# Kernel tuning notes

Measured on AMD Instinct MI355X. Metric: run time of the kernel, lower is better.

## Reference

```python
import jax, jax.numpy as jnp
import numpy as np

IN_DIM = 1024
OUT_DIM = 1024
NHEAD = 16
K = 9  # template(1032) - dim(1024) + 1


def _slinear(vec, template, conv_w, conv_b, lin_b):
    # Conv2d over template produces the [out_dim, in_dim] weight matrix.
    w = jax.lax.conv_general_dilated(
        template, conv_w, window_strides=(1, 1), padding='VALID',
        dimension_numbers=('NCHW', 'OIHW', 'NCHW'))  # [1,1,out_dim,in_dim]
    w = w[0, 0] + conv_b  # broadcast conv bias (scalar per out-channel)
    return vec @ w.T + lin_b  # F.linear(vec, w) + bias


def setup_inputs() -> dict:
    key = jax.random.key(0)
    ks = jax.random.split(key, 13)
    S, B = 2048, 2
    d = {
        'query': jax.random.normal(ks[0], (S, B, IN_DIM), jnp.float32),
        'key': jax.random.normal(ks[1], (S, B, IN_DIM), jnp.float32),
        'value': jax.random.normal(ks[2], (S, B, IN_DIM), jnp.float32),
        'template': jax.random.normal(ks[3], (1, 1, 1032, 1032), jnp.float32),
    }
    for i, name in enumerate(['wq', 'wk', 'wv']):
        d[name + '_cw'] = jax.random.normal(ks[4 + 3 * i], (1, 1, K, K), jnp.float32) * 0.05
        d[name + '_cb'] = jax.random.normal(ks[5 + 3 * i], (1,), jnp.float32) * 0.05
        d[name + '_b'] = jax.random.normal(ks[6 + 3 * i], (OUT_DIM,), jnp.float32) * 0.05
    return d


def reference(query, key, value, template,
              wq_cw, wq_cb, wq_b, wk_cw, wk_cb, wk_b, wv_cw, wv_cb, wv_b):
    q = _slinear(query, template, wq_cw, wq_cb, wq_b)
    k = _slinear(key, template, wk_cw, wk_cb, wk_b)
    v = _slinear(value, template, wv_cw, wv_cb, wv_b)
    S, B = q.shape[0], q.shape[1]
    h_dim = OUT_DIM // NHEAD
    scale = h_dim ** 0.5
    qh = q.reshape(S, B, NHEAD, h_dim)
    kh = k.reshape(S, B, NHEAD, h_dim)
    vh = v.reshape(S, B, NHEAD, h_dim)
    # batch_first=False path: scores then softmax over last dim
    scores = jnp.einsum('ibhd,jbhd->bhij', qh, kh) / scale  # [B,H,S,S]
    attn = jax.nn.softmax(scores, axis=-1)
    out = jnp.einsum('bhij,jbhd->ibhd', attn, vh).reshape(S, B, OUT_DIM)
    return out
```

## Files before the change

### kernel.cpp

```cpp
#include <hip/hip_runtime.h>
#include <math.h>

#define TDIM   1032
#define DIM    1024
#define SLEN   2048
#define BATCH  2
#define NROWS  (SLEN*BATCH)
#define NHEAD  16
#define HD     64

typedef unsigned short u16;
typedef short short8 __attribute__((ext_vector_type(8)));
typedef short bf16x4 __attribute__((ext_vector_type(4)));
typedef float f32x4  __attribute__((ext_vector_type(4)));

#define CSCALE 0.18033688011112042f

__device__ inline unsigned fbits(float x) {
    union { float f; unsigned u; } v; v.f = x; return v.u;
}
__device__ inline float asfloat(unsigned u) {
    union { unsigned u; float f; } v; v.u = u; return v.f;
}
__device__ inline u16 f2bf_rne(float x) {
    unsigned u = fbits(x);
    unsigned r = u + 0x7fffu + ((u >> 16) & 1u);
    return (u16)(r >> 16);
}
__device__ inline float bf2f(u16 b) { return asfloat(((unsigned)b) << 16); }
__device__ inline void dma16(const u16* g, u16* l) {
    __builtin_amdgcn_global_load_lds(
        (const __attribute__((address_space(1))) void*)g,
        (__attribute__((address_space(3))) void*)l, 16, 0, 0);
}

__global__ __launch_bounds__(256) void conv_weight_kernel(
    const float* __restrict__ tmpl,
    const float* __restrict__ cw0, const float* __restrict__ cb0,
    const float* __restrict__ cw1, const float* __restrict__ cb1,
    const float* __restrict__ cw2, const float* __restrict__ cb2,
    u16* __restrict__ Wh, u16* __restrict__ Wl)
{
    int t = blockIdx.z;
    const float* cw = (t == 0) ? cw0 : ((t == 1) ? cw1 : cw2);
    const float* cb = (t == 0) ? cb0 : ((t == 1) ? cb1 : cb2);
    __shared__ float scw[81];
    if (threadIdx.x < 81) scw[threadIdx.x] = cw[threadIdx.x];
    __syncthreads();
    int i = blockIdx.x * 256 + threadIdx.x;
    int o4 = blockIdx.y * 4;
    float cbv = cb[0];
    float acc[4] = {cbv, cbv, cbv, cbv};
    #pragma unroll
    for (int ry = 0; ry < 12; ++ry) {
        const float* trow = tmpl + (size_t)(o4 + ry) * TDIM + i;
        float tv[9];
        #pragma unroll
        for (int dx = 0; dx < 9; ++dx) tv[dx] = trow[dx];
        #pragma unroll
        for (int oo = 0; oo < 4; ++oo) {
            int dy = ry - oo;
            if (dy >= 0 && dy <= 8) {
                #pragma unroll
                for (int dx = 0; dx < 9; ++dx)
                    acc[oo] = fmaf(scw[dy * 9 + dx], tv[dx], acc[oo]);
            }
        }
    }
    #pragma unroll
    for (int oo = 0; oo < 4; ++oo) {
        size_t idx = (size_t)t * DIM * DIM + (size_t)(o4 + oo) * DIM + i;
        u16 h = f2bf_rne(acc[oo]);
        Wh[idx] = h;
        Wl[idx] = f2bf_rne(acc[oo] - bf2f(h));
    }
}

__global__ __launch_bounds__(256, 3) void qkv_mfma_gemm(
    const float* __restrict__ x0, const float* __restrict__ x1,
    const float* __restrict__ x2,
    const u16* __restrict__ Whg, const u16* __restrict__ Wlg,
    const float* __restrict__ b0, const float* __restrict__ b1,
    const float* __restrict__ b2,
    u16* __restrict__ Qh, u16* __restrict__ Ql,
    u16* __restrict__ Kh, u16* __restrict__ Kl,
    u16* __restrict__ Vb)
{
    unsigned flat = blockIdx.x + 8u * blockIdx.y + 256u * blockIdx.z;
    unsigned swz = (flat & 7u) * 96u + (flat >> 3);
    int t = swz >> 8;
    int n0 = (swz & 7u) * 128;
    int m0 = ((swz >> 3) & 31u) * 128;

    const float* X    = (t == 0) ? x0 : ((t == 1) ? x1 : x2);
    const u16* Bh_g   = Whg + (size_t)t * DIM * DIM;
    const u16* Bl_g   = Wlg + (size_t)t * DIM * DIM;
    const float* bias = (t == 0) ? b0 : ((t == 1) ? b1 : b2);

    __shared__ __align__(16) u16 lds[16384];
    u16* sAh = lds;
    u16* sAl = lds + 4096;
    u16* sBh = lds + 8192;
    u16* sBl = lds + 12288;

    int tid = threadIdx.x;
    int w = tid >> 6, lane = tid & 63;
    int c = lane & 15, quad = lane >> 4;
    int mh = (w >> 1) * 64, nh = (w & 1) * 64;

    int arow = w * 32 + (lane & 31);
    int acol = (lane >> 5) * 16;
    const float* aptr = X + (size_t)(m0 + arow) * DIM + acol;
    int awz = (arow >> 1) & 3;

    int srow = lane >> 2, sgr = lane & 3;
    int bsw = sgr ^ ((srow >> 1) & 3);

    f32x4 acc[4][4];
    #pragma unroll
    for (int i = 0; i < 4; ++i)
        #pragma unroll
        for (int j = 0; j < 4; ++j)
            #pragma unroll
            for (int r = 0; r < 4; ++r) acc[i][j][r] = 0.0f;

    float bias_v[4];
    #pragma unroll
    for (int tn = 0; tn < 4; ++tn) bias_v[tn] = bias[n0 + nh + tn * 16 + c];

    float4 xa[4];
    #pragma unroll
    for (int i = 0; i < 2; ++i) {
        int rb = w * 32 + i * 16;
        const u16* gh = Bh_g + (size_t)(n0 + rb + srow) * DIM + bsw * 8;
        const u16* gl = Bl_g + (size_t)(n0 + rb + srow) * DIM + bsw * 8;
        dma16(gh, sBh + rb * 32);
        dma16(gl, sBl + rb * 32);
    }
    #pragma unroll
    for (int j = 0; j < 4; ++j) xa[j] = *(const float4*)(aptr + j * 4);

    for (int it = 0; it < 32; ++it) {
        #pragma unroll
        for (int g = 0; g < 2; ++g) {
            float v[8] = { xa[2*g].x, xa[2*g].y, xa[2*g].z, xa[2*g].w,
                           xa[2*g+1].x, xa[2*g+1].y, xa[2*g+1].z, xa[2*g+1].w };
            short8 hv, lv;
            #pragma unroll
            for (int e = 0; e < 8; ++e) {
                unsigned u = fbits(v[e]);
                hv[e] = (short)(u >> 16);
                float l = v[e] - asfloat(u & 0xffff0000u);
                lv[e] = (short)(fbits(l) >> 16);
            }
            int chunk = (((lane >> 5) * 2 + g) ^ awz) * 8;
            *(short8*)(sAh + arow * 32 + chunk) = hv;
            *(short8*)(sAl + arow * 32 + chunk) = lv;
        }
        __syncthreads();

        short8 ah[4], al[4], bh[4], bl[4];
        int rsw = (quad ^ ((c >> 1) & 3)) * 8;
        #pragma unroll
        for (int tt = 0; tt < 4; ++tt) {
            int mi = (mh + tt * 16 + c) * 32 + rsw;
            ah[tt] = *(short8*)(sAh + mi);
            al[tt] = *(short8*)(sAl + mi);
            int ni = (nh + tt * 16 + c) * 32 + rsw;
            bh[tt] = *(short8*)(sBh + ni);
            bl[tt] = *(short8*)(sBl + ni);
        }
        __syncthreads();

        if (it < 31) {
            int kg = (it + 1) * 4;
            #pragma unroll
            for (int i = 0; i < 2; ++i) {
                int rb = w * 32 + i * 16;
                const u16* gh = Bh_g + (size_t)(n0 + rb + srow) * DIM + (kg + bsw) * 8;
                const u16* gl = Bl_g + (size_t)(n0 + rb + srow) * DIM + (kg + bsw) * 8;
                dma16(gh, sBh + rb * 32);
                dma16(gl, sBl + rb * 32);
            }
            #pragma unroll
            for (int j = 0; j < 4; ++j)
                xa[j] = *(const float4*)(aptr + (it + 1) * 32 + j * 4);
        }

        #pragma unroll
        for (int tm = 0; tm < 4; ++tm)
            #pragma unroll
            for (int tn = 0; tn < 4; ++tn) {
                acc[tm][tn] = __builtin_amdgcn_mfma_f32_16x16x32_bf16(
                    ah[tm], bh[tn], acc[tm][tn], 0, 0, 0);
                acc[tm][tn] = __builtin_amdgcn_mfma_f32_16x16x32_bf16(
                    ah[tm], bl[tn], acc[tm][tn], 0, 0, 0);
                acc[tm][tn] = __builtin_amdgcn_mfma_f32_16x16x32_bf16(
                    al[tm], bh[tn], acc[tm][tn], 0, 0, 0);
            }
    }

    if (t < 2) {
        u16* Yh = (t == 0) ? Qh : Kh;
        u16* Yl = (t == 0) ? Ql : Kl;
        float qs = (t == 0) ? CSCALE : 1.0f;
        #pragma unroll
        for (int tm = 0; tm < 4; ++tm)
            #pragma unroll
            for (int r = 0; r < 4; ++r) {
                int m = m0 + mh + tm * 16 + quad * 4 + r;
                #pragma unroll
                for (int tn = 0; tn < 4; ++tn) {
                    int n = n0 + nh + tn * 16 + c;
                    float o = (acc[tm][tn][r] + bias_v[tn]) * qs;
                    unsigned bo = fbits(o);
                    Yh[(size_t)m * DIM + n] = (u16)(bo >> 16);
                    float l = o - asfloat(bo & 0xffff0000u);
                    Yl[(size_t)m * DIM + n] = (u16)(fbits(l) >> 16);
                }
            }
    } else {
        #pragma unroll
        for (int tm = 0; tm < 4; ++tm)
            #pragma unroll
            for (int r = 0; r < 4; ++r) {
                int m = m0 + mh + tm * 16 + quad * 4 + r;
                #pragma unroll
                for (int tn = 0; tn < 4; ++tn) {
                    int n = n0 + nh + tn * 16 + c;
                    Vb[(size_t)m * DIM + n] =
                        (u16)(fbits(acc[tm][tn][r] + bias_v[tn]) >> 16);
                }
            }
    }
}

__global__ __launch_bounds__(256) void vt_kernel(
    const u16* __restrict__ Vb, u16* __restrict__ Vt)
{
    int b = blockIdx.z, h = blockIdx.y, s0 = blockIdx.x * 64;
    __shared__ __align__(16) u16 tile[64][80];
    int tid = threadIdx.x;
    int sl = tid >> 2, d0 = (tid & 3) * 16;
    const u16* src = Vb + (size_t)((s0 + sl) * BATCH + b) * DIM + h * HD + d0;
    short8 v0 = *(const short8*)src;
    short8 v1 = *(const short8*)(src + 8);
    #pragma unroll
    for (int j = 0; j < 8; ++j) {
        tile[d0 + j][sl] = (u16)v0[j];
        tile[d0 + 8 + j][sl] = (u16)v1[j];
    }
    __syncthreads();
    int d = tid >> 2, sc0 = (tid & 3) * 16;
    u16* dst = Vt + (size_t)((b * NHEAD + h) * HD + d) * SLEN + s0 + sc0;
    *(short8*)dst = *(const short8*)&tile[d][sc0];
    *(short8*)(dst + 8) = *(const short8*)&tile[d][sc0 + 8];
}

__global__ __launch_bounds__(512, 4) void attn_mfma_kernel(
    const u16* __restrict__ Qh, const u16* __restrict__ Ql,
    const u16* __restrict__ Kh, const u16* __restrict__ Kl,
    const u16* __restrict__ Vt, float* __restrict__ out)
{
    unsigned flat = blockIdx.x + 16u * blockIdx.y + 256u * blockIdx.z;
    unsigned swz = (flat & 7u) * 64u + (flat >> 3);
    int q0 = (swz & 15u) * 128;
    int h = (swz >> 4) & 15u;
    int b = swz >> 8;

    int tid = threadIdx.x;
    int w = tid >> 6, lane = tid & 63;
    int c = lane & 15, quad = lane >> 4;

    __shared__ __align__(16) u16 sbuf[2][3][4096];

    short8 qhf[2], qlf[2];
    {
        int s = q0 + w * 16 + c;
        size_t base = (size_t)(s * BATCH + b) * DIM + h * HD + quad * 8;
        qhf[0] = *(const short8*)(Qh + base);
        qhf[1] = *(const short8*)(Qh + base + 32);
        qlf[0] = *(const short8*)(Ql + base);
        qlf[1] = *(const short8*)(Ql + base + 32);
    }

    f32x4 acc[4];
    #pragma unroll
    for (int i = 0; i < 4; ++i)
        #pragma unroll
        for (int r = 0; r < 4; ++r) acc[i][r] = 0.0f;
    float m_run = -1e38f, l_run = 0.0f;

    int r3 = lane >> 3, c3 = lane & 7;
    int sw = c3 ^ r3;
    const size_t bhofs = (size_t)(b * NHEAD + h) * HD;

    #define ISSUE_DMA(n0v, bufv) do {                                          \
        int row_ = w * 8 + r3;                                                 \
        size_t gk = (size_t)(((n0v) + row_) * BATCH + b) * DIM + h * HD + sw * 8; \
        dma16(Kh + gk, &sbuf[bufv][0][w * 512]);                               \
        dma16(Kl + gk, &sbuf[bufv][1][w * 512]);                               \
        size_t gv = (bhofs + row_) * SLEN + (n0v) + sw * 8;                    \
        dma16(Vt + gv, &sbuf[bufv][2][w * 512]);                               \
    } while (0)

    ISSUE_DMA(0, 0);

    for (int it = 0; it < 32; ++it) {
        int cur = it & 1;
        __syncthreads();
        if (it < 31) ISSUE_DMA((it + 1) * 64, cur ^ 1);

        const u16* bKh = sbuf[cur][0];
        const u16* bKl = sbuf[cur][1];
        const u16* bVt = sbuf[cur][2];

        f32x4 sc[4];
        #pragma unroll
        for (int ct = 0; ct < 4; ++ct) {
            int row = ct * 16 + c, rw = row & 7;
            int kb = row * 64;
            short8 kh0 = *(const short8*)(bKh + kb + ((quad ^ rw) * 8));
            short8 kh1 = *(const short8*)(bKh + kb + (((4 + quad) ^ rw) * 8));
            short8 kl0 = *(const short8*)(bKl + kb + ((quad ^ rw) * 8));
            short8 kl1 = *(const short8*)(bKl + kb + (((4 + quad) ^ rw) * 8));
            __builtin_amdgcn_s_setprio(1);
            f32x4 s = {0.0f, 0.0f, 0.0f, 0.0f};
            s = __builtin_amdgcn_mfma_f32_16x16x32_bf16(kh0, qhf[0], s, 0, 0, 0);
            s = __builtin_amdgcn_mfma_f32_16x16x32_bf16(kh1, qhf[1], s, 0, 0, 0);
            s = __builtin_amdgcn_mfma_f32_16x16x32_bf16(kh0, qlf[0], s, 0, 0, 0);
            s = __builtin_amdgcn_mfma_f32_16x16x32_bf16(kh1, qlf[1], s, 0, 0, 0);
            s = __builtin_amdgcn_mfma_f32_16x16x32_bf16(kl0, qhf[0], s, 0, 0, 0);
            s = __builtin_amdgcn_mfma_f32_16x16x32_bf16(kl1, qhf[1], s, 0, 0, 0);
            __builtin_amdgcn_s_setprio(0);
            sc[ct] = s;
        }

        short8 vv[4][2];
        #pragma unroll
        for (int ctd = 0; ctd < 4; ++ctd) {
            int vrow = ctd * 16 + c, vrw = vrow & 7;
            int vb = vrow * 64;
            vv[ctd][0] = *(const short8*)(bVt + vb + ((quad ^ vrw) * 8));
            vv[ctd][1] = *(const short8*)(bVt + vb + (((4 + quad) ^ vrw) * 8));
        }

        short8 pf0, pf1;
        {
            float pm = sc[0][0];
            #pragma unroll
            for (int ct = 0; ct < 4; ++ct)
                #pragma unroll
                for (int r = 0; r < 4; ++r)
                    pm = fmaxf(pm, sc[ct][r]);
            pm = fmaxf(pm, __shfl_xor(pm, 16));
            pm = fmaxf(pm, __shfl_xor(pm, 32));
            float mnew = fmaxf(m_run, pm);
            bool noresc = __all(pm <= m_run);
            if (!noresc) {
                float al = exp2f(m_run - mnew);
                float alr[4];
                #pragma unroll
                for (int r = 0; r < 4; ++r)
                    alr[r] = __shfl(al, (lane & 48) | (quad * 4 + r));
                #pragma unroll
                for (int ctd = 0; ctd < 4; ++ctd)
                    #pragma unroll
                    for (int r = 0; r < 4; ++r) acc[ctd][r] *= alr[r];
                l_run *= al;
            }
            m_run = mnew;

            float ps = 0.0f;
            unsigned pw[8];
            #pragma unroll
            for (int ct = 0; ct < 4; ++ct) {
                float p0 = exp2f(sc[ct][0] - mnew);
                float p1 = exp2f(sc[ct][1] - mnew);
                float p2 = exp2f(sc[ct][2] - mnew);
                float p3 = exp2f(sc[ct][3] - mnew);
                ps += (p0 + p1) + (p2 + p3);
                pw[2*ct]   = (fbits(p0) >> 16) | (fbits(p1) & 0xffff0000u);
                pw[2*ct+1] = (fbits(p2) >> 16) | (fbits(p3) & 0xffff0000u);
            }
            ps += __shfl_xor(ps, 16);
            ps += __shfl_xor(ps, 32);
            l_run += ps;

            int sl0 = c + ((quad & 1) << 5);
            int sl1 = sl0 + 16;
            int sel = quad >> 1;
            union W8 { unsigned wv[4]; short8 s8; } f0, f1;
            {
                unsigned a0 = __shfl(pw[0], sl0), a1 = __shfl(pw[2], sl0);
                f0.wv[0] = sel ? a1 : a0;
                unsigned b0 = __shfl(pw[1], sl0), b1 = __shfl(pw[3], sl0);
                f0.wv[1] = sel ? b1 : b0;
                unsigned c0 = __shfl(pw[0], sl1), c1 = __shfl(pw[2], sl1);
                f0.wv[2] = sel ? c1 : c0;
                unsigned d0 = __shfl(pw[1], sl1), d1 = __shfl(pw[3], sl1);
                f0.wv[3] = sel ? d1 : d0;
                unsigned e0 = __shfl(pw[4], sl0), e1 = __shfl(pw[6], sl0);
                f1.wv[0] = sel ? e1 : e0;
                unsigned g0 = __shfl(pw[5], sl0), g1 = __shfl(pw[7], sl0);
                f1.wv[1] = sel ? g1 : g0;
                unsigned h0 = __shfl(pw[4], sl1), h1 = __shfl(pw[6], sl1);
                f1.wv[2] = sel ? h1 : h0;
                unsigned i0 = __shfl(pw[5], sl1), i1 = __shfl(pw[7], sl1);
                f1.wv[3] = sel ? i1 : i0;
            }
            pf0 = f0.s8;
            pf1 = f1.s8;
        }

        __builtin_amdgcn_s_setprio(1);
        #pragma unroll
        for (int ctd = 0; ctd < 4; ++ctd) {
            acc[ctd] = __builtin_amdgcn_mfma_f32_16x16x32_bf16(
                pf0, vv[ctd][0], acc[ctd], 0, 0, 0);
            acc[ctd] = __builtin_amdgcn_mfma_f32_16x16x32_bf16(
                pf1, vv[ctd][1], acc[ctd], 0, 0, 0);
        }
        __builtin_amdgcn_s_setprio(0);
    }
    #undef ISSUE_DMA

    {
        float rl[4];
        #pragma unroll
        for (int r = 0; r < 4; ++r)
            rl[r] = 1.0f / __shfl(l_run, (lane & 48) | (quad * 4 + r));
        #pragma unroll
        for (int ctd = 0; ctd < 4; ++ctd)
            #pragma unroll
            for (int r = 0; r < 4; ++r) {
                int s = q0 + w * 16 + quad * 4 + r;
                out[(size_t)(s * BATCH + b) * DIM + h * HD + ctd * 16 + c] =
                    acc[ctd][r] * rl[r];
            }
    }
}

extern "C" void kernel_launch(void* const* d_in, const int* in_sizes, int n_in,
                              void* d_out, int out_size, void* d_ws, size_t ws_size,
                              hipStream_t stream)
{
    const float* query = (const float*)d_in[0];
    const float* key_  = (const float*)d_in[1];
    const float* value = (const float*)d_in[2];
    const float* tmpl  = (const float*)d_in[3];
    const float* wq_cw = (const float*)d_in[4];
    const float* wq_cb = (const float*)d_in[5];
    const float* wq_b  = (const float*)d_in[6];
    const float* wk_cw = (const float*)d_in[7];
    const float* wk_cb = (const float*)d_in[8];
    const float* wk_b  = (const float*)d_in[9];
    const float* wv_cw = (const float*)d_in[10];
    const float* wv_cb = (const float*)d_in[11];
    const float* wv_b  = (const float*)d_in[12];

    char* ws = (char*)d_ws;
    u16* Wh = (u16*)(ws);
    u16* Wl = (u16*)(ws + 6291456);
    u16* Qh = (u16*)(ws + 12582912);
    u16* Ql = (u16*)(ws + 20971520);
    u16* Kh = (u16*)(ws + 29360128);
    u16* Kl = (u16*)(ws + 37748736);
    u16* Vb = (u16*)(ws + 46137344);
    u16* Vt = (u16*)(ws + 54525952);
    float* out = (float*)d_out;

    conv_weight_kernel<<<dim3(DIM / 256, DIM / 4, 3), 256, 0, stream>>>(
        tmpl, wq_cw, wq_cb, wk_cw, wk_cb, wv_cw, wv_cb, Wh, Wl);

    qkv_mfma_gemm<<<dim3(DIM / 128, NROWS / 128, 3), 256, 0, stream>>>(
        query, key_, value, Wh, Wl, wq_b, wk_b, wv_b, Qh, Ql, Kh, Kl, Vb);

    vt_kernel<<<dim3(SLEN / 64, NHEAD, BATCH), 256, 0, stream>>>(Vb, Vt);

    attn_mfma_kernel<<<dim3(SLEN / 128, NHEAD, BATCH), 512, 0, stream>>>(
        Qh, Ql, Kh, Kl, Vt, out);
}
```

Baseline: 315.1 us.

## Pre-split activations into bf16 hi/lo buffers before the QKV GEMM

Adds a separate kernel that converts the fp32 query/key/value activations once into bf16 high and low halves in workspace. A new GEMM variant then loads both A and B tiles with direct 16-byte copies into LDS instead of converting fp32 inside the GEMM. This removes repeated per-tile conversion work and the fp32 A traffic from the GEMM, at the cost of an extra kernel launch and about 48 MB of extra global writes and reads. The path is used only when the workspace is large enough, otherwise the old GEMM runs.

```diff
diff --git a/kernel.cpp b/kernel.cpp
--- a/kernel.cpp
+++ b/kernel.cpp
@@ -76,7 +76,161 @@
     }
 }
 
-__global__ __launch_bounds__(256, 3) void qkv_mfma_gemm(
+__global__ __launch_bounds__(256) void xsplit_kernel(
+    const float* __restrict__ x0, const float* __restrict__ x1,
+    const float* __restrict__ x2,
+    u16* __restrict__ Xh, u16* __restrict__ Xl)
+{
+    int t = blockIdx.y;
+    const float* X = (t == 0) ? x0 : ((t == 1) ? x1 : x2);
+    u16* oh = Xh + (size_t)t * NROWS * DIM;
+    u16* ol = Xl + (size_t)t * NROWS * DIM;
+    size_t base = ((size_t)blockIdx.x * 256 + threadIdx.x) * 8;
+    float4 a = *(const float4*)(X + base);
+    float4 b = *(const float4*)(X + base + 4);
+    float v[8] = {a.x, a.y, a.z, a.w, b.x, b.y, b.z, b.w};
+    short8 hv, lv;
+    #pragma unroll
+    for (int e = 0; e < 8; ++e) {
+        unsigned u = fbits(v[e]);
+        hv[e] = (short)(u >> 16);
+        float l = v[e] - asfloat(u & 0xffff0000u);
+        lv[e] = (short)(fbits(l) >> 16);
+    }
+    *(short8*)(oh + base) = hv;
+    *(short8*)(ol + base) = lv;
+}
+
+__global__ __launch_bounds__(256, 3) void qkv_mfma_gemm_ps(
+    const u16* __restrict__ Xhg, const u16* __restrict__ Xlg,
+    const u16* __restrict__ Whg, const u16* __restrict__ Wlg,
+    const float* __restrict__ b0, const float* __restrict__ b1,
+    const float* __restrict__ b2,
+    u16* __restrict__ Qh, u16* __restrict__ Ql,
+    u16* __restrict__ Kh, u16* __restrict__ Kl,
+    u16* __restrict__ Vb)
+{
+    unsigned flat = blockIdx.x + 8u * blockIdx.y + 256u * blockIdx.z;
+    unsigned swz = (flat & 7u) * 96u + (flat >> 3);
+    int t = swz >> 8;
+    int n0 = (swz & 7u) * 128;
+    int m0 = ((swz >> 3) & 31u) * 128;
+
+    const u16* Ah_g = Xhg + (size_t)t * NROWS * DIM;
+    const u16* Al_g = Xlg + (size_t)t * NROWS * DIM;
+    const u16* Bh_g = Whg + (size_t)t * DIM * DIM;
+    const u16* Bl_g = Wlg + (size_t)t * DIM * DIM;
+    const float* bias = (t == 0) ? b0 : ((t == 1) ? b1 : b2);
+
+    __shared__ __align__(16) u16 lds[16384];
+    u16* sAh = lds;
+    u16* sAl = lds + 4096;
+    u16* sBh = lds + 8192;
+    u16* sBl = lds + 12288;
+
+    int tid = threadIdx.x;
+    int w = tid >> 6, lane = tid & 63;
+    int c = lane & 15, quad = lane >> 4;
+    int mh = (w >> 1) * 64, nh = (w & 1) * 64;
+
+    int srow = lane >> 2, sgr = lane & 3;
+    int ssw = sgr ^ ((srow >> 1) & 3);
+
+    f32x4 acc[4][4];
+    #pragma unroll
+    for (int i = 0; i < 4; ++i)
+        #pragma unroll
+        for (int j = 0; j < 4; ++j)
+            #pragma unroll
+            for (int r = 0; r < 4; ++r) acc[i][j][r] = 0.0f;
+
+    float bias_v[4];
+    #pragma unroll
+    for (int tn = 0; tn < 4; ++tn) bias_v[tn] = bias[n0 + nh + tn * 16 + c];
+
+    #define STAGE(kg) do {                                                     \
+        _Pragma("unroll")                                                      \
+        for (int i_ = 0; i_ < 2; ++i_) {                                       \
+            int rb = w * 32 + i_ * 16;                                         \
+            size_t ro = (size_t)(n0 + rb + srow) * DIM + ((kg) + ssw) * 8;     \
+            dma16(Bh_g + ro, sBh + rb * 32);                                   \
+            dma16(Bl_g + ro, sBl + rb * 32);                                   \
+            size_t ao = (size_t)(m0 + rb + srow) * DIM + ((kg) + ssw) * 8;     \
+            dma16(Ah_g + ao, sAh + rb * 32);                                   \
+            dma16(Al_g + ao, sAl + rb * 32);                                   \
+        }                                                                      \
+    } while (0)
+
+    STAGE(0);
+
+    for (int it = 0; it < 32; ++it) {
+        __syncthreads();
+
+        short8 ah[4], al[4], bh[4], bl[4];
+        int rsw = (quad ^ ((c >> 1) & 3)) * 8;
+        #pragma unroll
+        for (int tt = 0; tt < 4; ++tt) {
+            int mi = (mh + tt * 16 + c) * 32 + rsw;
+            ah[tt] = *(short8*)(sAh + mi);
+            al[tt] = *(short8*)(sAl + mi);
+            int ni = (nh + tt * 16 + c) * 32 + rsw;
+            bh[tt] = *(short8*)(sBh + ni);
+            bl[tt] = *(short8*)(sBl + ni);
+        }
+        __syncthreads();
+
+        if (it < 31) STAGE((it + 1) * 4);
+
+        #pragma unroll
+        for (int tm = 0; tm < 4; ++tm)
+            #pragma unroll
+            for (int tn = 0; tn < 4; ++tn) {
+                acc[tm][tn] = __builtin_amdgcn_mfma_f32_16x16x32_bf16(
+                    ah[tm], bh[tn], acc[tm][tn], 0, 0, 0);
+                acc[tm][tn] = __builtin_amdgcn_mfma_f32_16x16x32_bf16(
+                    ah[tm], bl[tn], acc[tm][tn], 0, 0, 0);
+                acc[tm][tn] = __builtin_amdgcn_mfma_f32_16x16x32_bf16(
+                    al[tm], bh[tn], acc[tm][tn], 0, 0, 0);
+            }
+    }
+    #undef STAGE
+
+    if (t < 2) {
+        u16* Yh = (t == 0) ? Qh : Kh;
+        u16* Yl = (t == 0) ? Ql : Kl;
+        float qs = (t == 0) ? CSCALE : 1.0f;
+        #pragma unroll
+        for (int tm = 0; tm < 4; ++tm)
+            #pragma unroll
+            for (int r = 0; r < 4; ++r) {
+                int m = m0 + mh + tm * 16 + quad * 4 + r;
+                #pragma unroll
+                for (int tn = 0; tn < 4; ++tn) {
+                    int n = n0 + nh + tn * 16 + c;
+                    float o = (acc[tm][tn][r] + bias_v[tn]) * qs;
+                    unsigned bo = fbits(o);
+                    Yh[(size_t)m * DIM + n] = (u16)(bo >> 16);
+                    float l = o - asfloat(bo & 0xffff0000u);
+                    Yl[(size_t)m * DIM + n] = (u16)(fbits(l) >> 16);
+                }
+            }
+    } else {
+        #pragma unroll
+        for (int tm = 0; tm < 4; ++tm)
+            #pragma unroll
+            for (int r = 0; r < 4; ++r) {
+                int m = m0 + mh + tm * 16 + quad * 4 + r;
+                #pragma unroll
+                for (int tn = 0; tn < 4; ++tn) {
+                    int n = n0 + nh + tn * 16 + c;
+                    Vb[(size_t)m * DIM + n] =
+                        (u16)(fbits(acc[tm][tn][r] + bias_v[tn]) >> 16);
+                }
+            }
+    }
+}
+
+__global__ __launch_bounds__(256, 3) void qkv_mfma_gemm_fb(
     const float* __restrict__ x0, const float* __restrict__ x1,
     const float* __restrict__ x2,
     const u16* __restrict__ Whg, const u16* __restrict__ Wlg,
@@ -468,13 +622,24 @@
     u16* Kl = (u16*)(ws + 37748736);
     u16* Vb = (u16*)(ws + 46137344);
     u16* Vt = (u16*)(ws + 54525952);
+    u16* Xh = (u16*)(ws + 62914560);
+    u16* Xl = (u16*)(ws + 88080384);
     float* out = (float*)d_out;
+
+    bool presplit = ws_size >= 113246208ull;
 
     conv_weight_kernel<<<dim3(DIM / 256, DIM / 4, 3), 256, 0, stream>>>(
         tmpl, wq_cw, wq_cb, wk_cw, wk_cb, wv_cw, wv_cb, Wh, Wl);
 
-    qkv_mfma_gemm<<<dim3(DIM / 128, NROWS / 128, 3), 256, 0, stream>>>(
-        query, key_, value, Wh, Wl, wq_b, wk_b, wv_b, Qh, Ql, Kh, Kl, Vb);
+    if (presplit) {
+        xsplit_kernel<<<dim3(NROWS * DIM / (256 * 8), 3), 256, 0, stream>>>(
+            query, key_, value, Xh, Xl);
+        qkv_mfma_gemm_ps<<<dim3(DIM / 128, NROWS / 128, 3), 256, 0, stream>>>(
+            Xh, Xl, Wh, Wl, wq_b, wk_b, wv_b, Qh, Ql, Kh, Kl, Vb);
+    } else {
+        qkv_mfma_gemm_fb<<<dim3(DIM / 128, NROWS / 128, 3), 256, 0, stream>>>(
+            query, key_, value, Wh, Wl, wq_b, wk_b, wv_b, Qh, Ql, Kh, Kl, Vb);
+    }
 
     vt_kernel<<<dim3(SLEN / 64, NHEAD, BATCH), 256, 0, stream>>>(Vb, Vt);
 
```

Measured after the change: 303.2 us. 1.04x faster.
